# Kernel optimization log

Hardware: AMD Instinct MI355X
Metric: run time of the kernel (lower is better)

The kernel has to match this reference:

```python
import jax, jax.numpy as jnp
import numpy as np

DN = ('NCDHW', 'OIDHW', 'NCDHW')
HIDDEN = 512
VOCAB = 8192


def conv3d_s122(x, w, b):
    # stride (1,2,2), padding 1 on all three spatial-temporal dims
    y = jax.lax.conv_general_dilated(x, w, window_strides=(1, 2, 2),
                                     padding=[(1, 1), (1, 1), (1, 1)],
                                     dimension_numbers=DN)
    return y + b[None, :, None, None, None]


def setup_inputs() -> dict:
    key = jax.random.key(0)
    ks = jax.random.split(key, 9)
    c1, c2 = HIDDEN // 4, HIDDEN // 2
    inp = {
        'video': jax.random.normal(ks[0], (2, 3, 16, 128, 128), dtype=jnp.float32),
        'w1': jax.random.normal(ks[1], (c1, 3, 3, 3, 3), dtype=jnp.float32) * 0.05,
        'b1': jnp.zeros((c1,), dtype=jnp.float32),
        'w2': jax.random.normal(ks[2], (c2, c1, 3, 3, 3), dtype=jnp.float32) * 0.05,
        'b2': jnp.zeros((c2,), dtype=jnp.float32),
        'w3': jax.random.normal(ks[3], (HIDDEN, c2, 3, 3, 3), dtype=jnp.float32) * 0.05,
        'b3': jnp.zeros((HIDDEN,), dtype=jnp.float32),
        'codebook': jax.random.normal(ks[4], (VOCAB, HIDDEN), dtype=jnp.float32),
        'emb_table': jax.random.normal(ks[5], (VOCAB, HIDDEN), dtype=jnp.float32),
        'resolution_level': 0,
    }
    return inp


def reference(video, w1, b1, w2, b2, w3, b3, codebook, emb_table, resolution_level):
    h = jax.nn.relu(conv3d_s122(video, w1, b1))
    h = jax.nn.relu(conv3d_s122(h, w2, b2))
    f = conv3d_s122(h, w3, b3)                       # [B, C, T, H', W']
    B, C = f.shape[0], f.shape[1]
    feats = f.reshape(B, C, -1).transpose(0, 2, 1)   # [B, N, C]
    # squared L2 distances (argmin identical to cdist's sqrt distances)
    f2 = jnp.sum(feats * feats, axis=-1, keepdims=True)          # [B, N, 1]
    c2 = jnp.sum(codebook * codebook, axis=-1)                   # [V]
    dots = jnp.einsum('bnc,vc->bnv', feats, codebook)            # [B, N, V]
    sqdist = f2 + c2[None, None, :] - 2.0 * dots
    tokens = jnp.argmin(sqdist, axis=-1)                         # [B, N] int
    embeddings = emb_table[tokens]                               # [B, N, C]
    return tokens, embeddings
```

## Files before the change

### kernel.cpp

```cpp
#include <hip/hip_runtime.h>

typedef __bf16 bf16x8 __attribute__((ext_vector_type(8)));
typedef float  f32x4  __attribute__((ext_vector_type(4)));

__device__ __forceinline__ unsigned int splitpack(float x) {
  unsigned int u = __float_as_uint(x);
  unsigned int hi = (u + 0x7fffu + ((u >> 16) & 1u)) >> 16;
  float l = x - __uint_as_float(hi << 16);
  unsigned int ul = __float_as_uint(l);
  unsigned int lo = (ul + 0x7fffu + ((ul >> 16) & 1u)) >> 16;
  return hi | (lo << 16);
}

__device__ __forceinline__ void mfma_bf16(f32x4& d, uint4 a, uint4 b) {
  d = __builtin_amdgcn_mfma_f32_16x16x32_bf16(
        __builtin_bit_cast(bf16x8, a), __builtin_bit_cast(bf16x8, b), d, 0, 0, 0);
}


__global__ void conv1_k(const float* __restrict__ in, const float* __restrict__ wgt,
                        const float* __restrict__ bias, unsigned int* __restrict__ h1p) {
  const int tx = threadIdx.x;
  const int w0 = tx * 4;
  const int h  = blockIdx.x * 16 + threadIdx.y;
  const int co0 = blockIdx.y * 8;
  const int bz = blockIdx.z;
  const int b = bz >> 4, t = bz & 15;

  float acc[8][4];
  #pragma unroll
  for (int i = 0; i < 8; ++i) {
    const float bv = bias[co0 + i];
    #pragma unroll
    for (int j = 0; j < 4; ++j) acc[i][j] = bv;
  }
  const int cs = 2 * w0 - 2;

  for (int ci = 0; ci < 3; ++ci) {
    const float* inc = in + (size_t)((b * 3 + ci) * 16) * (128 * 128);
    const float* wc  = wgt + ((size_t)co0 * 3 + ci) * 27;
    #pragma unroll
    for (int kd = 0; kd < 3; ++kd) {
      const int t2 = t - 1 + kd;
      if (t2 < 0 || t2 >= 16) continue;
      const float* ip = inc + t2 * (128 * 128);
      #pragma unroll
      for (int kh = 0; kh < 3; ++kh) {
        const int hh = 2 * h - 1 + kh;
        float v[10];
        if (hh >= 0) {
          const float* r = ip + hh * 128 + cs;
          if (cs >= 0) { float2 u = *(const float2*)r; v[0] = u.x; v[1] = u.y; }
          else         { v[0] = 0.f; v[1] = 0.f; }
          float2 u1 = *(const float2*)(r + 2); v[2] = u1.x; v[3] = u1.y;
          float2 u2 = *(const float2*)(r + 4); v[4] = u2.x; v[5] = u2.y;
          float2 u3 = *(const float2*)(r + 6); v[6] = u3.x; v[7] = u3.y;
          float2 u4 = *(const float2*)(r + 8); v[8] = u4.x; v[9] = u4.y;
        } else {
          #pragma unroll
          for (int z = 0; z < 10; ++z) v[z] = 0.f;
        }
        #pragma unroll
        for (int i = 0; i < 8; ++i) {
          const float* wp = wc + (size_t)i * (3 * 27) + kd * 9 + kh * 3;
          const float wa = wp[0], wb = wp[1], wcc = wp[2];
          #pragma unroll
          for (int wi = 0; wi < 4; ++wi) {
            acc[i][wi] = fmaf(v[1 + 2*wi], wa,  acc[i][wi]);
            acc[i][wi] = fmaf(v[2 + 2*wi], wb,  acc[i][wi]);
            acc[i][wi] = fmaf(v[3 + 2*wi], wcc, acc[i][wi]);
          }
        }
      }
    }
  }
  const int ph = h & 1, rr = h >> 1, cc0 = tx * 2;
  const size_t base0 = (size_t)b * 8388608 + (size_t)blockIdx.y * 524288
                     + (size_t)t * 32768 + (size_t)(ph * 2) * 8192 + (size_t)rr * 256;
  #pragma unroll
  for (int i = 0; i < 8; ++i) {
    unsigned int p0 = splitpack(fmaxf(acc[i][0], 0.f));
    unsigned int p1 = splitpack(fmaxf(acc[i][1], 0.f));
    unsigned int p2 = splitpack(fmaxf(acc[i][2], 0.f));
    unsigned int p3 = splitpack(fmaxf(acc[i][3], 0.f));
    h1p[base0 + cc0 * 8 + i]              = p0;
    h1p[base0 + 8192 + cc0 * 8 + i]       = p1;
    h1p[base0 + (cc0 + 1) * 8 + i]        = p2;
    h1p[base0 + 8192 + (cc0 + 1) * 8 + i] = p3;
  }
}

__global__ void split_w2_k(const float* __restrict__ w2, unsigned short* __restrict__ whi,
                           unsigned short* __restrict__ wlo) {
  unsigned int o = blockIdx.x * 256u + threadIdx.x;
  unsigned int j   = o & 7u;
  unsigned int col = (o >> 3) & 127u;
  unsigned int kg  = (o >> 10) & 3u;
  unsigned int cbk = (o >> 12) & 1u;
  unsigned int cic = (o >> 13) & 3u;
  unsigned int tap = o >> 15;
  unsigned int co = cbk * 128u + col, ci = cic * 32u + kg * 8u + j;
  float x = w2[((size_t)co * 128u + ci) * 27u + tap];
  unsigned int p = splitpack(x);
  whi[o] = (unsigned short)(p & 0xffffu);
  wlo[o] = (unsigned short)(p >> 16);
}

__global__ void split_w3_k(const float* __restrict__ w3, unsigned short* __restrict__ whi,
                           unsigned short* __restrict__ wlo) {
  unsigned int o = blockIdx.x * 256u + threadIdx.x;
  unsigned int j   = o & 7u;
  unsigned int col = (o >> 3) & 127u;
  unsigned int kg  = (o >> 10) & 3u;
  unsigned int cb  = (o >> 12) & 3u;
  unsigned int cic = (o >> 14) & 7u;
  unsigned int tap = o >> 17;
  unsigned int co = cb * 128u + col, ci = cic * 32u + kg * 8u + j;
  float x = w3[((size_t)co * 256u + ci) * 27u + tap];
  unsigned int p = splitpack(x);
  whi[o] = (unsigned short)(p & 0xffffu);
  wlo[o] = (unsigned short)(p >> 16);
}

__global__ void split_cb_k(const float* __restrict__ cb, unsigned short* __restrict__ cbhi,
                           unsigned short* __restrict__ cblo) {
  unsigned int o = blockIdx.x * 256u + threadIdx.x;
  unsigned int j   = o & 7u;
  unsigned int row = (o >> 3) & 127u;
  unsigned int kq  = (o >> 10) & 3u;
  unsigned int kc  = (o >> 12) & 15u;
  unsigned int vb  = o >> 16;
  unsigned int v = vb * 128u + row, k = kc * 32u + kq * 8u + j;
  float x = cb[(size_t)v * 512u + k];
  unsigned int p = splitpack(x);
  cbhi[o] = (unsigned short)(p & 0xffffu);
  cblo[o] = (unsigned short)(p >> 16);
}

__global__ void c2_k(const float* __restrict__ cb, float* __restrict__ c2) {
  const int wid = threadIdx.x >> 6, lane = threadIdx.x & 63;
  const int v = blockIdx.x * 4 + wid;
  const float* row = cb + (size_t)v * 512 + lane * 8;
  float4 a = *(const float4*)row, b = *(const float4*)(row + 4);
  float s = a.x*a.x + a.y*a.y + a.z*a.z + a.w*a.w
          + b.x*b.x + b.y*b.y + b.z*b.z + b.w*b.w;
  #pragma unroll
  for (int off = 32; off; off >>= 1) s += __shfl_down(s, off);
  if (lane == 0) c2[v] = s;
}

#define NCH2 108
#define BUFO 16384
__global__ __launch_bounds__(512) void conv2_mfma_k(
    const unsigned int* __restrict__ xp,
    const unsigned short* __restrict__ whi, const unsigned short* __restrict__ wlo,
    const float* __restrict__ bias,
    unsigned int* __restrict__ h2p) {
  __shared__ __align__(16) unsigned short lds[32768];

  const int tid  = threadIdx.x;
  const int lane = tid & 63;
  const int wid  = tid >> 6;
  const int wm   = wid >> 2, wn = wid & 3;
  const int bid = blockIdx.x;
  const int xcd = bid & 7;
  const int q   = bid >> 3;
  const int cbk = q & 1;
  const int nb  = (q >> 1) & 7;
  const int bt  = xcd + 8 * (q >> 4);
  const int b = bt >> 4, t = bt & 15;

  const int skg = tid >> 7;
  const int sn  = tid & 127;
  const int s_hout = nb * 4 + (sn >> 5);
  const int s_wout = sn & 31;

  const int lc = lane & 15, kgl = lane >> 4;

  f32x4 acc[4][2];
  #pragma unroll
  for (int mf = 0; mf < 4; ++mf)
    #pragma unroll
    for (int nf = 0; nf < 2; ++nf) acc[mf][nf] = (f32x4)(0.f);

  auto issue = [&](int ic, uint4& xa, uint4& xb, uint4& wh, uint4& wl) {
    const int tap = ic >> 2, cic = ic & 3;
    const int kd = tap / 9, r9 = tap % 9;
    const int kh = r9 / 3, kw = r9 % 3;
    const int tt = t + kd - 1;
    const int pl = ((kh != 1) ? 2 : 0) + ((kw != 1) ? 1 : 0);
    const int r  = s_hout + (kh != 0) - 1;
    const int c  = s_wout + (kw != 0) - 1;
    const bool oob = (tt < 0) || (tt > 15) || (r < 0) || (c < 0);
    const int o = b * 8388608 + (cic * 4 + skg) * 524288 + tt * 32768 + pl * 8192 + (r * 32 + c) * 8;
    const unsigned int* src = xp + (oob ? 0 : o);
    uint4 a = *(const uint4*)src, bb = *(const uint4*)(src + 4);
    if (oob) { a = make_uint4(0u,0u,0u,0u); bb = make_uint4(0u,0u,0u,0u); }
    xa = a; xb = bb;
    const size_t slab = ((size_t)((tap * 4 + cic) * 2 + cbk)) << 12;
    wh = *(const uint4*)(whi + slab + tid * 8);
    wl = *(const uint4*)(wlo + slab + tid * 8);
  };

  auto stage = [&](int bo, const uint4& xa, const uint4& xb, const uint4& wh, const uint4& wl) {
    *(uint4*)&lds[bo + tid * 8] = wh;
    *(uint4*)&lds[bo + 4096 + tid * 8] = wl;
    uint4 H, L;
    H.x = (xa.x & 0xffffu) | (xa.y << 16);  L.x = (xa.x >> 16) | (xa.y & 0xffff0000u);
    H.y = (xa.z & 0xffffu) | (xa.w << 16);  L.y = (xa.z >> 16) | (xa.w & 0xffff0000u);
    H.z = (xb.x & 0xffffu) | (xb.y << 16);  L.z = (xb.x >> 16) | (xb.y & 0xffff0000u);
    H.w = (xb.z & 0xffffu) | (xb.w << 16);  L.w = (xb.z >> 16) | (xb.w & 0xffff0000u);
    *(uint4*)&lds[bo + 8192  + (skg * 128 + sn) * 8] = H;
    *(uint4*)&lds[bo + 12288 + (skg * 128 + sn) * 8] = L;
  };

  auto mma = [&](int bo) {
    uint4 ah[4], al[4], bh[2], bl[2];
    #pragma unroll
    for (int mf = 0; mf < 4; ++mf) {
      const int o = bo + kgl * 1024 + (wm * 64 + mf * 16 + lc) * 8;
      ah[mf] = *(const uint4*)&lds[o];
      al[mf] = *(const uint4*)&lds[o + 4096];
    }
    #pragma unroll
    for (int nf = 0; nf < 2; ++nf) {
      const int o = bo + 8192 + kgl * 1024 + (wn * 32 + nf * 16 + lc) * 8;
      bh[nf] = *(const uint4*)&lds[o];
      bl[nf] = *(const uint4*)&lds[o + 4096];
    }
    #pragma unroll
    for (int mf = 0; mf < 4; ++mf)
      #pragma unroll
      for (int nf = 0; nf < 2; ++nf) mfma_bf16(acc[mf][nf], ah[mf], bh[nf]);
    #pragma unroll
    for (int mf = 0; mf < 4; ++mf)
      #pragma unroll
      for (int nf = 0; nf < 2; ++nf) mfma_bf16(acc[mf][nf], ah[mf], bl[nf]);
    #pragma unroll
    for (int mf = 0; mf < 4; ++mf)
      #pragma unroll
      for (int nf = 0; nf < 2; ++nf) mfma_bf16(acc[mf][nf], al[mf], bh[nf]);
  };

  uint4 xa0, xb0, wh0, wl0, xa1, xb1, wh1, wl1;
  issue(0, xa0, xb0, wh0, wl0);
  issue(1, xa1, xb1, wh1, wl1);

  #pragma unroll 1
  for (int ic = 0; ic < NCH2; ic += 2) {
    stage(0, xa0, xb0, wh0, wl0);
    __syncthreads();
    if (ic + 2 < NCH2) issue(ic + 2, xa0, xb0, wh0, wl0);
    mma(0);
    stage(BUFO, xa1, xb1, wh1, wl1);
    __syncthreads();
    if (ic + 3 < NCH2) issue(ic + 3, xa1, xb1, wh1, wl1);
    mma(BUFO);
  }

  const int lr4 = (lane >> 4) * 4;
  #pragma unroll
  for (int mf = 0; mf < 4; ++mf) {
    const int co0g = cbk * 128 + wm * 64 + mf * 16 + lr4;
    const float4 bv = *(const float4*)(bias + co0g);
    const float* bp = (const float*)&bv;
    const size_t gbase = (size_t)(b * 32 + (co0g >> 3)) * 131072 + (size_t)t * 8192 + (co0g & 7);
    #pragma unroll
    for (int nf = 0; nf < 2; ++nf) {
      const int n_l = wn * 32 + nf * 16 + lc;
      const int h_out = nb * 4 + (n_l >> 5);
      const int w_out = n_l & 31;
      const int pl_o = ((h_out & 1) << 1) | (w_out & 1);
      const size_t sp = gbase + (size_t)pl_o * 2048 + (size_t)((h_out >> 1) * 16 + (w_out >> 1)) * 8;
      #pragma unroll
      for (int r = 0; r < 4; ++r) {
        const float x = fmaxf(acc[mf][nf][r] + bp[r], 0.f);
        h2p[sp + r] = splitpack(x);
      }
    }
  }
}

#define NCH 216
__global__ __launch_bounds__(512) void conv3_mfma_k(
    const unsigned int* __restrict__ xp,
    const unsigned short* __restrict__ whi, const unsigned short* __restrict__ wlo,
    const float* __restrict__ bias,
    unsigned short* __restrict__ fhi, unsigned short* __restrict__ flo) {
  __shared__ __align__(16) unsigned short lds[32768];

  const int tid  = threadIdx.x;
  const int lane = tid & 63;
  const int wid  = tid >> 6;
  const int wm   = wid >> 2, wn = wid & 3;
  const int bid = blockIdx.x;
  const int xcd = bid & 7;
  const int q   = bid >> 3;
  const int cb  = q & 3;
  const int hb  = (q >> 2) & 1;
  const int bt  = xcd + 8 * (q >> 3);
  const int b = bt >> 4, t = bt & 15;

  const int skg = tid >> 7;
  const int sn  = tid & 127;
  const int shn = hb * 8 + (sn >> 4);
  const int swn = sn & 15;

  const int lc = lane & 15, kgl = lane >> 4;

  f32x4 acc[4][2];
  #pragma unroll
  for (int mf = 0; mf < 4; ++mf)
    #pragma unroll
    for (int nf = 0; nf < 2; ++nf) acc[mf][nf] = (f32x4)(0.f);

  auto issue = [&](int ic, uint4& xa, uint4& xb, uint4& wh, uint4& wl) {
    const int tap = ic >> 3, cic = ic & 7;
    const int kd = tap / 9, r9 = tap % 9;
    const int kh = r9 / 3, kw = r9 % 3;
    const int tt = t + kd - 1;
    const int pl = ((kh != 1) ? 2 : 0) + ((kw != 1) ? 1 : 0);
    const int r  = shn + (kh != 0) - 1;
    const int c  = swn + (kw != 0) - 1;
    const bool oob = (tt < 0) || (tt > 15) || (r < 0) || (c < 0);
    const int o = b * 4194304 + (cic * 4 + skg) * 131072 + tt * 8192 + pl * 2048 + (r * 16 + c) * 8;
    const unsigned int* src = xp + (oob ? 0 : o);
    uint4 a = *(const uint4*)src, bb = *(const uint4*)(src + 4);
    if (oob) { a = make_uint4(0u,0u,0u,0u); bb = make_uint4(0u,0u,0u,0u); }
    xa = a; xb = bb;
    const size_t slab = ((size_t)((tap * 8 + cic) * 4 + cb)) << 12;
    wh = *(const uint4*)(whi + slab + tid * 8);
    wl = *(const uint4*)(wlo + slab + tid * 8);
  };

  auto stage = [&](int bo, const uint4& xa, const uint4& xb, const uint4& wh, const uint4& wl) {
    *(uint4*)&lds[bo + tid * 8] = wh;
    *(uint4*)&lds[bo + 4096 + tid * 8] = wl;
    uint4 H, L;
    H.x = (xa.x & 0xffffu) | (xa.y << 16);  L.x = (xa.x >> 16) | (xa.y & 0xffff0000u);
    H.y = (xa.z & 0xffffu) | (xa.w << 16);  L.y = (xa.z >> 16) | (xa.w & 0xffff0000u);
    H.z = (xb.x & 0xffffu) | (xb.y << 16);  L.z = (xb.x >> 16) | (xb.y & 0xffff0000u);
    H.w = (xb.z & 0xffffu) | (xb.w << 16);  L.w = (xb.z >> 16) | (xb.w & 0xffff0000u);
    *(uint4*)&lds[bo + 8192  + (skg * 128 + sn) * 8] = H;
    *(uint4*)&lds[bo + 12288 + (skg * 128 + sn) * 8] = L;
  };

  auto mma = [&](int bo) {
    uint4 ah[4], al[4], bh[2], bl[2];
    #pragma unroll
    for (int mf = 0; mf < 4; ++mf) {
      const int o = bo + kgl * 1024 + (wm * 64 + mf * 16 + lc) * 8;
      ah[mf] = *(const uint4*)&lds[o];
      al[mf] = *(const uint4*)&lds[o + 4096];
    }
    #pragma unroll
    for (int nf = 0; nf < 2; ++nf) {
      const int o = bo + 8192 + kgl * 1024 + (wn * 32 + nf * 16 + lc) * 8;
      bh[nf] = *(const uint4*)&lds[o];
      bl[nf] = *(const uint4*)&lds[o + 4096];
    }
    #pragma unroll
    for (int mf = 0; mf < 4; ++mf)
      #pragma unroll
      for (int nf = 0; nf < 2; ++nf) mfma_bf16(acc[mf][nf], ah[mf], bh[nf]);
    #pragma unroll
    for (int mf = 0; mf < 4; ++mf)
      #pragma unroll
      for (int nf = 0; nf < 2; ++nf) mfma_bf16(acc[mf][nf], ah[mf], bl[nf]);
    #pragma unroll
    for (int mf = 0; mf < 4; ++mf)
      #pragma unroll
      for (int nf = 0; nf < 2; ++nf) mfma_bf16(acc[mf][nf], al[mf], bh[nf]);
  };

  uint4 xa0, xb0, wh0, wl0, xa1, xb1, wh1, wl1;
  issue(0, xa0, xb0, wh0, wl0);
  issue(1, xa1, xb1, wh1, wl1);

  #pragma unroll 1
  for (int ic = 0; ic < NCH; ic += 2) {
    stage(0, xa0, xb0, wh0, wl0);
    __syncthreads();
    if (ic + 2 < NCH) issue(ic + 2, xa0, xb0, wh0, wl0);
    mma(0);
    stage(BUFO, xa1, xb1, wh1, wl1);
    __syncthreads();
    if (ic + 3 < NCH) issue(ic + 3, xa1, xb1, wh1, wl1);
    mma(BUFO);
  }

  const int lr4 = (lane >> 4) * 4;
  const int tokb = b * 32 + t * 2 + hb;
  #pragma unroll
  for (int mf = 0; mf < 4; ++mf) {
    const int co0g = cb * 128 + wm * 64 + mf * 16 + lr4;
    const float4 bv = *(const float4*)(bias + co0g);
    const int kc = co0g >> 5, kq = (co0g >> 3) & 3, j0 = co0g & 7;
    #pragma unroll
    for (int nf = 0; nf < 2; ++nf) {
      const int n_l = wn * 32 + nf * 16 + lc;
      const size_t off = (size_t)(tokb * 16 + kc) * 4096 + kq * 1024 + n_l * 8 + j0;
      unsigned int p0 = splitpack(acc[mf][nf][0] + bv.x);
      unsigned int p1 = splitpack(acc[mf][nf][1] + bv.y);
      unsigned int p2 = splitpack(acc[mf][nf][2] + bv.z);
      unsigned int p3 = splitpack(acc[mf][nf][3] + bv.w);
      ushort4 h4, l4;
      h4.x = (unsigned short)(p0 & 0xffffu); l4.x = (unsigned short)(p0 >> 16);
      h4.y = (unsigned short)(p1 & 0xffffu); l4.y = (unsigned short)(p1 >> 16);
      h4.z = (unsigned short)(p2 & 0xffffu); l4.z = (unsigned short)(p2 >> 16);
      h4.w = (unsigned short)(p3 & 0xffffu); l4.w = (unsigned short)(p3 >> 16);
      *(ushort4*)(fhi + off) = h4;
      *(ushort4*)(flo + off) = l4;
    }
  }
}

__global__ __launch_bounds__(512) void vq_mfma_k(
    const unsigned short* __restrict__ fhi, const unsigned short* __restrict__ flo,
    const unsigned short* __restrict__ cbhi, const unsigned short* __restrict__ cblo,
    const float* __restrict__ c2,
    float* __restrict__ pval, int* __restrict__ pidx) {
  __shared__ __align__(16) unsigned short lds[16384];

  const int tid  = threadIdx.x;
  const int lane = tid & 63;
  const int wid  = tid >> 6;
  const int wm   = wid >> 2, wn = wid & 3;
  const int vb = blockIdx.x;
  const int tb = blockIdx.y;
  const int v0 = vb * 128, tok0 = tb * 128;

  const int lc = lane & 15, kgl = lane >> 4;
  const uint4* pAhi[4]; const uint4* pAlo[4];
  #pragma unroll
  for (int mf = 0; mf < 4; ++mf) {
    const int off = kgl * 1024 + (wm * 64 + mf * 16 + lc) * 8;
    pAhi[mf] = (const uint4*)&lds[off];
    pAlo[mf] = (const uint4*)&lds[4096 + off];
  }
  const uint4* pBhi[2]; const uint4* pBlo[2];
  #pragma unroll
  for (int nf = 0; nf < 2; ++nf) {
    const int off = kgl * 1024 + (wn * 32 + nf * 16 + lc) * 8;
    pBhi[nf] = (const uint4*)&lds[8192 + off];
    pBlo[nf] = (const uint4*)&lds[12288 + off];
  }
  uint4* wAhi = (uint4*)&lds[tid * 8];
  uint4* wAlo = (uint4*)&lds[4096 + tid * 8];
  uint4* wBhi = (uint4*)&lds[8192 + tid * 8];
  uint4* wBlo = (uint4*)&lds[12288 + tid * 8];

  f32x4 acc[4][2];
  #pragma unroll
  for (int mf = 0; mf < 4; ++mf)
    #pragma unroll
    for (int nf = 0; nf < 2; ++nf) acc[mf][nf] = (f32x4)(0.f);

  uint4 cah, cal, fbh, fbl;
  auto issue = [&](int kc) {
    const size_t cboff = (size_t)(vb * 16 + kc) * 4096 + tid * 8;
    const size_t foff  = (size_t)(tb * 16 + kc) * 4096 + tid * 8;
    cah = *(const uint4*)(cbhi + cboff);
    cal = *(const uint4*)(cblo + cboff);
    fbh = *(const uint4*)(fhi + foff);
    fbl = *(const uint4*)(flo + foff);
  };

  issue(0);

  for (int kc = 0; kc < 16; ++kc) {
    __syncthreads();
    *wAhi = cah;
    *wAlo = cal;
    *wBhi = fbh;
    *wBlo = fbl;
    __syncthreads();
    if (kc + 1 < 16) issue(kc + 1);

    uint4 ah[4], al[4], bh[2], bl[2];
    #pragma unroll
    for (int mf = 0; mf < 4; ++mf) { ah[mf] = *pAhi[mf]; al[mf] = *pAlo[mf]; }
    #pragma unroll
    for (int nf = 0; nf < 2; ++nf) { bh[nf] = *pBhi[nf]; bl[nf] = *pBlo[nf]; }

    #pragma unroll
    for (int mf = 0; mf < 4; ++mf)
      #pragma unroll
      for (int nf = 0; nf < 2; ++nf) mfma_bf16(acc[mf][nf], ah[mf], bh[nf]);
    #pragma unroll
    for (int mf = 0; mf < 4; ++mf)
      #pragma unroll
      for (int nf = 0; nf < 2; ++nf) mfma_bf16(acc[mf][nf], ah[mf], bl[nf]);
    #pragma unroll
    for (int mf = 0; mf < 4; ++mf)
      #pragma unroll
      for (int nf = 0; nf < 2; ++nf) mfma_bf16(acc[mf][nf], al[mf], bh[nf]);
  }

  float best[2]; int bidx[2];
  best[0] = best[1] = 3.4e38f; bidx[0] = bidx[1] = 0;
  #pragma unroll
  for (int mf = 0; mf < 4; ++mf) {
    float cc[4];
    *(float4*)cc = *(const float4*)(c2 + v0 + wm * 64 + mf * 16 + kgl * 4);
    #pragma unroll
    for (int nf = 0; nf < 2; ++nf) {
      #pragma unroll
      for (int r = 0; r < 4; ++r) {
        const float d = cc[r] - 2.f * acc[mf][nf][r];
        const int vg = v0 + wm * 64 + mf * 16 + kgl * 4 + r;
        if (d < best[nf] || (d == best[nf] && vg < bidx[nf])) { best[nf] = d; bidx[nf] = vg; }
      }
    }
  }
  #pragma unroll
  for (int off = 16; off <= 32; off <<= 1) {
    #pragma unroll
    for (int nf = 0; nf < 2; ++nf) {
      const float ov = __shfl_xor(best[nf], off);
      const int   oi = __shfl_xor(bidx[nf], off);
      if (ov < best[nf] || (ov == best[nf] && oi < bidx[nf])) { best[nf] = ov; bidx[nf] = oi; }
    }
  }
  if (lane < 16) {
    #pragma unroll
    for (int nf = 0; nf < 2; ++nf) {
      const int tok = tok0 + wn * 32 + nf * 16 + lane;
      const int slot = vb * 2 + wm;
      pval[(size_t)tok * 128 + slot] = best[nf];
      pidx[(size_t)tok * 128 + slot] = bidx[nf];
    }
  }
}

__global__ void vq_reduce_k(const float* __restrict__ pval, const int* __restrict__ pidx,
                            int* __restrict__ tokens, float* __restrict__ out_tok) {
  const int tok = blockIdx.x * blockDim.x + threadIdx.x;
  float best = 3.4e38f; int bi = 0;
  for (int s = 0; s < 128; ++s) {
    const float v = pval[(size_t)tok * 128 + s];
    const int idx = pidx[(size_t)tok * 128 + s];
    if (v < best || (v == best && idx < bi)) { best = v; bi = idx; }
  }
  tokens[tok] = bi;
  out_tok[tok] = (float)bi;
}

__global__ void gather_k(const int* __restrict__ tokens, const float* __restrict__ emb,
                         float* __restrict__ out) {
  const int i = blockIdx.x * blockDim.x + threadIdx.x;
  const int n = i >> 7;
  const int c4 = (i & 127) * 4;
  const int tk = tokens[n];
  float4 v = *(const float4*)(emb + (size_t)tk * 512 + c4);
  *(float4*)(out + (size_t)n * 512 + c4) = v;
}

extern "C" void kernel_launch(void* const* d_in, const int* in_sizes, int n_in,
                              void* d_out, int out_size, void* d_ws, size_t ws_size,
                              hipStream_t stream) {
  const float* video = (const float*)d_in[0];
  const float* w1 = (const float*)d_in[1];
  const float* b1 = (const float*)d_in[2];
  const float* w2 = (const float*)d_in[3];
  const float* b2 = (const float*)d_in[4];
  const float* w3 = (const float*)d_in[5];
  const float* b3 = (const float*)d_in[6];
  const float* cb  = (const float*)d_in[7];
  const float* emb = (const float*)d_in[8];

  float* ws = (float*)d_ws;
  unsigned int* h1p = (unsigned int*)ws;
  unsigned short* fhi = (unsigned short*)(ws);
  unsigned short* flo = (unsigned short*)(ws + 2097152);
  unsigned short* cbhi = (unsigned short*)(ws + 4194304);
  unsigned short* cblo = (unsigned short*)(ws + 6291456);
  float* c2v  = ws + 8388608;
  float* pval = ws + 8396800;
  int*   pidx = (int*)(ws + 9445376);
  int*   tokens = (int*)(ws + 10493952);
  unsigned int* h2p = (unsigned int*)(ws + 16777216);
  unsigned short* w2hi = (unsigned short*)d_out;
  unsigned short* w2lo = w2hi + 884736;
  unsigned short* w3hi = (unsigned short*)d_out;
  unsigned short* w3lo = w3hi + 3538944;
  float* out_tok = (float*)d_out;
  float* out_emb = (float*)d_out + 8192;

  hipLaunchKernelGGL(conv1_k, dim3(4, 16, 32), dim3(16, 16), 0, stream, video, w1, b1, h1p);
  hipLaunchKernelGGL(split_w2_k, dim3(3456), dim3(256), 0, stream, w2, w2hi, w2lo);
  hipLaunchKernelGGL(conv2_mfma_k, dim3(512), dim3(512), 0, stream,
                     h1p, w2hi, w2lo, b2, h2p);
  hipLaunchKernelGGL(split_w3_k, dim3(13824), dim3(256), 0, stream, w3, w3hi, w3lo);
  hipLaunchKernelGGL(split_cb_k, dim3(16384), dim3(256), 0, stream, cb, cbhi, cblo);
  hipLaunchKernelGGL(c2_k, dim3(2048), dim3(256), 0, stream, cb, c2v);
  hipLaunchKernelGGL(conv3_mfma_k, dim3(256), dim3(512), 0, stream,
                     h2p, w3hi, w3lo, b3, fhi, flo);
  hipLaunchKernelGGL(vq_mfma_k, dim3(64, 64), dim3(512), 0, stream,
                     fhi, flo, cbhi, cblo, c2v, pval, pidx);
  hipLaunchKernelGGL(vq_reduce_k, dim3(32), dim3(256), 0, stream, pval, pidx, tokens, out_tok);
  hipLaunchKernelGGL(gather_k, dim3(4096), dim3(256), 0, stream, tokens, emb, out_emb);
}
```

Measured before the change: 749.7 us.

## Split conv3 output-channel tiles into 64-wide blocks for more workgroups

The conv3 MFMA kernel changes from 256 blocks of 512 threads, each computing 128 output channels, to 512 blocks of 256 threads, each computing 64 output channels. Each thread now stages two activation vectors. Weight staging, the LDS layout and the index math are reworked to match, with a smaller double-buffered LDS footprint. The goal is to fill more CUs, since 256 blocks underfill the device, and to allow two blocks per CU. The cost is that every activation tile is loaded by twice as many blocks, which raises global and LDS traffic.

```diff
diff --git a/kernel.cpp b/kernel.cpp
--- a/kernel.cpp
+++ b/kernel.cpp
@@ -282,29 +282,31 @@
 }
 
 #define NCH 216
-__global__ __launch_bounds__(512) void conv3_mfma_k(
+#define BUF3 12288
+__global__ __launch_bounds__(256, 2) void conv3_mfma_k(
     const unsigned int* __restrict__ xp,
     const unsigned short* __restrict__ whi, const unsigned short* __restrict__ wlo,
     const float* __restrict__ bias,
     unsigned short* __restrict__ fhi, unsigned short* __restrict__ flo) {
-  __shared__ __align__(16) unsigned short lds[32768];
+  __shared__ __align__(16) unsigned short lds[24576];
 
   const int tid  = threadIdx.x;
   const int lane = tid & 63;
-  const int wid  = tid >> 6;
-  const int wm   = wid >> 2, wn = wid & 3;
+  const int wn   = tid >> 6;
   const int bid = blockIdx.x;
   const int xcd = bid & 7;
   const int q   = bid >> 3;
-  const int cb  = q & 3;
-  const int hb  = (q >> 2) & 1;
-  const int bt  = xcd + 8 * (q >> 3);
+  const int cb8 = q & 7;
+  const int hb  = (q >> 3) & 1;
+  const int bt  = xcd + 8 * (q >> 4);
   const int b = bt >> 4, t = bt & 15;
 
-  const int skg = tid >> 7;
-  const int sn  = tid & 127;
-  const int shn = hb * 8 + (sn >> 4);
-  const int swn = sn & 15;
+  const int stok = tid & 127;
+  const int skg  = tid >> 7;
+  const int shn = hb * 8 + (stok >> 4);
+  const int swn = stok & 15;
+  const int cb = cb8 >> 1, cb64 = (cb8 & 1) * 64;
+  const int woff = ((tid >> 6) * 128 + cb64 + (tid & 63)) * 8;
 
   const int lc = lane & 15, kgl = lane >> 4;
 
@@ -314,7 +316,8 @@
     #pragma unroll
     for (int nf = 0; nf < 2; ++nf) acc[mf][nf] = (f32x4)(0.f);
 
-  auto issue = [&](int ic, uint4& xa, uint4& xb, uint4& wh, uint4& wl) {
+  auto issue = [&](int ic, uint4& x0a, uint4& x0b, uint4& x1a, uint4& x1b,
+                   uint4& wh, uint4& wl) {
     const int tap = ic >> 3, cic = ic & 7;
     const int kd = tap / 9, r9 = tap % 9;
     const int kh = r9 / 3, kw = r9 % 3;
@@ -323,39 +326,52 @@
     const int r  = shn + (kh != 0) - 1;
     const int c  = swn + (kw != 0) - 1;
     const bool oob = (tt < 0) || (tt > 15) || (r < 0) || (c < 0);
-    const int o = b * 4194304 + (cic * 4 + skg) * 131072 + tt * 8192 + pl * 2048 + (r * 16 + c) * 8;
-    const unsigned int* src = xp + (oob ? 0 : o);
-    uint4 a = *(const uint4*)src, bb = *(const uint4*)(src + 4);
-    if (oob) { a = make_uint4(0u,0u,0u,0u); bb = make_uint4(0u,0u,0u,0u); }
-    xa = a; xb = bb;
+    const int o0 = b * 4194304 + (cic * 4 + skg) * 131072 + tt * 8192 + pl * 2048 + (r * 16 + c) * 8;
+    const unsigned int* s0 = xp + (oob ? 0 : o0);
+    const unsigned int* s1 = xp + (oob ? 0 : (o0 + 262144));
+    uint4 a0 = *(const uint4*)s0, b0 = *(const uint4*)(s0 + 4);
+    uint4 a1 = *(const uint4*)s1, b1 = *(const uint4*)(s1 + 4);
+    if (oob) {
+      a0 = make_uint4(0u,0u,0u,0u); b0 = make_uint4(0u,0u,0u,0u);
+      a1 = make_uint4(0u,0u,0u,0u); b1 = make_uint4(0u,0u,0u,0u);
+    }
+    x0a = a0; x0b = b0; x1a = a1; x1b = b1;
     const size_t slab = ((size_t)((tap * 8 + cic) * 4 + cb)) << 12;
-    wh = *(const uint4*)(whi + slab + tid * 8);
-    wl = *(const uint4*)(wlo + slab + tid * 8);
+    wh = *(const uint4*)(whi + slab + woff);
+    wl = *(const uint4*)(wlo + slab + woff);
   };
 
-  auto stage = [&](int bo, const uint4& xa, const uint4& xb, const uint4& wh, const uint4& wl) {
+  auto stage = [&](int bo, const uint4& x0a, const uint4& x0b,
+                   const uint4& x1a, const uint4& x1b,
+                   const uint4& wh, const uint4& wl) {
     *(uint4*)&lds[bo + tid * 8] = wh;
-    *(uint4*)&lds[bo + 4096 + tid * 8] = wl;
-    uint4 H, L;
-    H.x = (xa.x & 0xffffu) | (xa.y << 16);  L.x = (xa.x >> 16) | (xa.y & 0xffff0000u);
-    H.y = (xa.z & 0xffffu) | (xa.w << 16);  L.y = (xa.z >> 16) | (xa.w & 0xffff0000u);
-    H.z = (xb.x & 0xffffu) | (xb.y << 16);  L.z = (xb.x >> 16) | (xb.y & 0xffff0000u);
-    H.w = (xb.z & 0xffffu) | (xb.w << 16);  L.w = (xb.z >> 16) | (xb.w & 0xffff0000u);
-    *(uint4*)&lds[bo + 8192  + (skg * 128 + sn) * 8] = H;
-    *(uint4*)&lds[bo + 12288 + (skg * 128 + sn) * 8] = L;
+    *(uint4*)&lds[bo + 2048 + tid * 8] = wl;
+    uint4 H0, L0, H1, L1;
+    H0.x = (x0a.x & 0xffffu) | (x0a.y << 16);  L0.x = (x0a.x >> 16) | (x0a.y & 0xffff0000u);
+    H0.y = (x0a.z & 0xffffu) | (x0a.w << 16);  L0.y = (x0a.z >> 16) | (x0a.w & 0xffff0000u);
+    H0.z = (x0b.x & 0xffffu) | (x0b.y << 16);  L0.z = (x0b.x >> 16) | (x0b.y & 0xffff0000u);
+    H0.w = (x0b.z & 0xffffu) | (x0b.w << 16);  L0.w = (x0b.z >> 16) | (x0b.w & 0xffff0000u);
+    H1.x = (x1a.x & 0xffffu) | (x1a.y << 16);  L1.x = (x1a.x >> 16) | (x1a.y & 0xffff0000u);
+    H1.y = (x1a.z & 0xffffu) | (x1a.w << 16);  L1.y = (x1a.z >> 16) | (x1a.w & 0xffff0000u);
+    H1.z = (x1b.x & 0xffffu) | (x1b.y << 16);  L1.z = (x1b.x >> 16) | (x1b.y & 0xffff0000u);
+    H1.w = (x1b.z & 0xffffu) | (x1b.w << 16);  L1.w = (x1b.z >> 16) | (x1b.w & 0xffff0000u);
+    *(uint4*)&lds[bo + 4096 + tid * 8]          = H0;
+    *(uint4*)&lds[bo + 4096 + (tid + 256) * 8]  = H1;
+    *(uint4*)&lds[bo + 8192 + tid * 8]          = L0;
+    *(uint4*)&lds[bo + 8192 + (tid + 256) * 8]  = L1;
   };
 
   auto mma = [&](int bo) {
     uint4 ah[4], al[4], bh[2], bl[2];
     #pragma unroll
     for (int mf = 0; mf < 4; ++mf) {
-      const int o = bo + kgl * 1024 + (wm * 64 + mf * 16 + lc) * 8;
+      const int o = bo + kgl * 512 + (mf * 16 + lc) * 8;
       ah[mf] = *(const uint4*)&lds[o];
-      al[mf] = *(const uint4*)&lds[o + 4096];
+      al[mf] = *(const uint4*)&lds[o + 2048];
     }
     #pragma unroll
     for (int nf = 0; nf < 2; ++nf) {
-      const int o = bo + 8192 + kgl * 1024 + (wn * 32 + nf * 16 + lc) * 8;
+      const int o = bo + 4096 + kgl * 1024 + (wn * 32 + nf * 16 + lc) * 8;
       bh[nf] = *(const uint4*)&lds[o];
       bl[nf] = *(const uint4*)&lds[o + 4096];
     }
@@ -373,27 +389,28 @@
       for (int nf = 0; nf < 2; ++nf) mfma_bf16(acc[mf][nf], al[mf], bh[nf]);
   };
 
-  uint4 xa0, xb0, wh0, wl0, xa1, xb1, wh1, wl1;
-  issue(0, xa0, xb0, wh0, wl0);
-  issue(1, xa1, xb1, wh1, wl1);
+  uint4 p0xa, p0xb, p0ya, p0yb, p0wh, p0wl;
+  uint4 p1xa, p1xb, p1ya, p1yb, p1wh, p1wl;
+  issue(0, p0xa, p0xb, p0ya, p0yb, p0wh, p0wl);
+  issue(1, p1xa, p1xb, p1ya, p1yb, p1wh, p1wl);
 
   #pragma unroll 1
   for (int ic = 0; ic < NCH; ic += 2) {
-    stage(0, xa0, xb0, wh0, wl0);
+    stage(0, p0xa, p0xb, p0ya, p0yb, p0wh, p0wl);
     __syncthreads();
-    if (ic + 2 < NCH) issue(ic + 2, xa0, xb0, wh0, wl0);
+    if (ic + 2 < NCH) issue(ic + 2, p0xa, p0xb, p0ya, p0yb, p0wh, p0wl);
     mma(0);
-    stage(BUFO, xa1, xb1, wh1, wl1);
+    stage(BUF3, p1xa, p1xb, p1ya, p1yb, p1wh, p1wl);
     __syncthreads();
-    if (ic + 3 < NCH) issue(ic + 3, xa1, xb1, wh1, wl1);
-    mma(BUFO);
+    if (ic + 3 < NCH) issue(ic + 3, p1xa, p1xb, p1ya, p1yb, p1wh, p1wl);
+    mma(BUF3);
   }
 
   const int lr4 = (lane >> 4) * 4;
   const int tokb = b * 32 + t * 2 + hb;
   #pragma unroll
   for (int mf = 0; mf < 4; ++mf) {
-    const int co0g = cb * 128 + wm * 64 + mf * 16 + lr4;
+    const int co0g = cb8 * 64 + mf * 16 + lr4;
     const float4 bv = *(const float4*)(bias + co0g);
     const int kc = co0g >> 5, kq = (co0g >> 3) & 3, j0 = co0g & 7;
     #pragma unroll
@@ -594,7 +611,7 @@
   hipLaunchKernelGGL(split_w3_k, dim3(13824), dim3(256), 0, stream, w3, w3hi, w3lo);
   hipLaunchKernelGGL(split_cb_k, dim3(16384), dim3(256), 0, stream, cb, cbhi, cblo);
   hipLaunchKernelGGL(c2_k, dim3(2048), dim3(256), 0, stream, cb, c2v);
-  hipLaunchKernelGGL(conv3_mfma_k, dim3(256), dim3(512), 0, stream,
+  hipLaunchKernelGGL(conv3_mfma_k, dim3(512), dim3(256), 0, stream,
                      h2p, w3hi, w3lo, b3, fhi, flo);
   hipLaunchKernelGGL(vq_mfma_k, dim3(64, 64), dim3(512), 0, stream,
                      fhi, flo, cbhi, cblo, c2v, pval, pidx);
```

After: 749.1 us. About the same (-0.1%).

## Split conv3 reduction in two halves with atomic partial sums

Applied to the files above, without the earlier changes.

Conv3 now splits its 216-chunk K reduction into two halves, launching 512 blocks instead of 256. This gives more parallelism on a GPU with many compute units. Partial results are accumulated with float atomicAdd into a zeroed fp32 buffer. A separate combine kernel then adds the bias and performs the hi/lo bf16 split. This adds a zeroing kernel, a combine kernel, atomic traffic and extra memory round trips, and makes the float summation order nondeterministic.

```diff
diff --git a/kernel.cpp b/kernel.cpp
--- a/kernel.cpp
+++ b/kernel.cpp
@@ -281,12 +281,15 @@
   }
 }
 
-#define NCH 216
+__global__ void zero_f_k(float4* __restrict__ p) {
+  p[blockIdx.x * 256 + threadIdx.x] = make_float4(0.f, 0.f, 0.f, 0.f);
+}
+
+#define NCH3H 108
 __global__ __launch_bounds__(512) void conv3_mfma_k(
     const unsigned int* __restrict__ xp,
     const unsigned short* __restrict__ whi, const unsigned short* __restrict__ wlo,
-    const float* __restrict__ bias,
-    unsigned short* __restrict__ fhi, unsigned short* __restrict__ flo) {
+    float* __restrict__ fpart) {
   __shared__ __align__(16) unsigned short lds[32768];
 
   const int tid  = threadIdx.x;
@@ -298,8 +301,10 @@
   const int q   = bid >> 3;
   const int cb  = q & 3;
   const int hb  = (q >> 2) & 1;
-  const int bt  = xcd + 8 * (q >> 3);
+  const int kh2 = (q >> 3) & 1;
+  const int bt  = xcd + 8 * (q >> 4);
   const int b = bt >> 4, t = bt & 15;
+  const int koff = kh2 * NCH3H;
 
   const int skg = tid >> 7;
   const int sn  = tid & 127;
@@ -314,8 +319,8 @@
     #pragma unroll
     for (int nf = 0; nf < 2; ++nf) acc[mf][nf] = (f32x4)(0.f);
 
-  auto issue = [&](int ic, uint4& xa, uint4& xb, uint4& wh, uint4& wl) {
-    const int tap = ic >> 3, cic = ic & 7;
+  auto issue = [&](int chunk, uint4& xa, uint4& xb, uint4& wh, uint4& wl) {
+    const int tap = chunk >> 3, cic = chunk & 7;
     const int kd = tap / 9, r9 = tap % 9;
     const int kh = r9 / 3, kw = r9 % 3;
     const int tt = t + kd - 1;
@@ -374,18 +379,18 @@
   };
 
   uint4 xa0, xb0, wh0, wl0, xa1, xb1, wh1, wl1;
-  issue(0, xa0, xb0, wh0, wl0);
-  issue(1, xa1, xb1, wh1, wl1);
+  issue(koff + 0, xa0, xb0, wh0, wl0);
+  issue(koff + 1, xa1, xb1, wh1, wl1);
 
   #pragma unroll 1
-  for (int ic = 0; ic < NCH; ic += 2) {
+  for (int ic = 0; ic < NCH3H; ic += 2) {
     stage(0, xa0, xb0, wh0, wl0);
     __syncthreads();
-    if (ic + 2 < NCH) issue(ic + 2, xa0, xb0, wh0, wl0);
+    if (ic + 2 < NCH3H) issue(koff + ic + 2, xa0, xb0, wh0, wl0);
     mma(0);
     stage(BUFO, xa1, xb1, wh1, wl1);
     __syncthreads();
-    if (ic + 3 < NCH) issue(ic + 3, xa1, xb1, wh1, wl1);
+    if (ic + 3 < NCH3H) issue(koff + ic + 3, xa1, xb1, wh1, wl1);
     mma(BUFO);
   }
 
@@ -394,25 +399,39 @@
   #pragma unroll
   for (int mf = 0; mf < 4; ++mf) {
     const int co0g = cb * 128 + wm * 64 + mf * 16 + lr4;
-    const float4 bv = *(const float4*)(bias + co0g);
     const int kc = co0g >> 5, kq = (co0g >> 3) & 3, j0 = co0g & 7;
     #pragma unroll
     for (int nf = 0; nf < 2; ++nf) {
       const int n_l = wn * 32 + nf * 16 + lc;
       const size_t off = (size_t)(tokb * 16 + kc) * 4096 + kq * 1024 + n_l * 8 + j0;
-      unsigned int p0 = splitpack(acc[mf][nf][0] + bv.x);
-      unsigned int p1 = splitpack(acc[mf][nf][1] + bv.y);
-      unsigned int p2 = splitpack(acc[mf][nf][2] + bv.z);
-      unsigned int p3 = splitpack(acc[mf][nf][3] + bv.w);
-      ushort4 h4, l4;
-      h4.x = (unsigned short)(p0 & 0xffffu); l4.x = (unsigned short)(p0 >> 16);
-      h4.y = (unsigned short)(p1 & 0xffffu); l4.y = (unsigned short)(p1 >> 16);
-      h4.z = (unsigned short)(p2 & 0xffffu); l4.z = (unsigned short)(p2 >> 16);
-      h4.w = (unsigned short)(p3 & 0xffffu); l4.w = (unsigned short)(p3 >> 16);
-      *(ushort4*)(fhi + off) = h4;
-      *(ushort4*)(flo + off) = l4;
-    }
-  }
+      #pragma unroll
+      for (int r = 0; r < 4; ++r)
+        atomicAdd(&fpart[off + r], acc[mf][nf][r]);
+    }
+  }
+}
+
+__global__ void combine_f_k(const float* __restrict__ fpart, const float* __restrict__ bias,
+                            unsigned short* __restrict__ fhi, unsigned short* __restrict__ flo) {
+  const unsigned int i0 = (blockIdx.x * 256u + threadIdx.x) * 4u;
+  const unsigned int within = i0 & 4095u;
+  const unsigned int kc = (i0 >> 12) & 15u;
+  const unsigned int kq = within >> 10;
+  const unsigned int j0 = within & 7u;
+  const unsigned int co0 = kc * 32u + kq * 8u + j0;
+  const float4 p = *(const float4*)(fpart + i0);
+  const float4 bv = *(const float4*)(bias + co0);
+  unsigned int q0 = splitpack(p.x + bv.x);
+  unsigned int q1 = splitpack(p.y + bv.y);
+  unsigned int q2 = splitpack(p.z + bv.z);
+  unsigned int q3 = splitpack(p.w + bv.w);
+  ushort4 h4, l4;
+  h4.x = (unsigned short)(q0 & 0xffffu); l4.x = (unsigned short)(q0 >> 16);
+  h4.y = (unsigned short)(q1 & 0xffffu); l4.y = (unsigned short)(q1 >> 16);
+  h4.z = (unsigned short)(q2 & 0xffffu); l4.z = (unsigned short)(q2 >> 16);
+  h4.w = (unsigned short)(q3 & 0xffffu); l4.w = (unsigned short)(q3 >> 16);
+  *(ushort4*)(fhi + i0) = h4;
+  *(ushort4*)(flo + i0) = l4;
 }
 
 __global__ __launch_bounds__(512) void vq_mfma_k(
@@ -579,6 +598,7 @@
   float* pval = ws + 8396800;
   int*   pidx = (int*)(ws + 9445376);
   int*   tokens = (int*)(ws + 10493952);
+  float* fpart = ws + 10502144;
   unsigned int* h2p = (unsigned int*)(ws + 16777216);
   unsigned short* w2hi = (unsigned short*)d_out;
   unsigned short* w2lo = w2hi + 884736;
@@ -594,8 +614,10 @@
   hipLaunchKernelGGL(split_w3_k, dim3(13824), dim3(256), 0, stream, w3, w3hi, w3lo);
   hipLaunchKernelGGL(split_cb_k, dim3(16384), dim3(256), 0, stream, cb, cbhi, cblo);
   hipLaunchKernelGGL(c2_k, dim3(2048), dim3(256), 0, stream, cb, c2v);
-  hipLaunchKernelGGL(conv3_mfma_k, dim3(256), dim3(512), 0, stream,
-                     h2p, w3hi, w3lo, b3, fhi, flo);
+  hipLaunchKernelGGL(zero_f_k, dim3(4096), dim3(256), 0, stream, (float4*)fpart);
+  hipLaunchKernelGGL(conv3_mfma_k, dim3(512), dim3(512), 0, stream,
+                     h2p, w3hi, w3lo, fpart);
+  hipLaunchKernelGGL(combine_f_k, dim3(4096), dim3(256), 0, stream, fpart, b3, fhi, flo);
   hipLaunchKernelGGL(vq_mfma_k, dim3(64, 64), dim3(512), 0, stream,
                      fhi, flo, cbhi, cblo, c2v, pval, pidx);
   hipLaunchKernelGGL(vq_reduce_k, dim3(32), dim3(256), 0, stream, pval, pidx, tokens, out_tok);
```

Result: slower. 797.5 us (+6.4%).
